# Kernel optimization log

Hardware: AMD Instinct MI355X
Metric: run time of the kernel (lower is better)

## Reference

```python
import jax, jax.numpy as jnp
import numpy as np
from jax.scipy.special import digamma

K = 3
N_CLASSES = 10
HIGH_CST = 1e7


def setup_inputs() -> dict:
    key = jax.random.key(0)
    k1, k2 = jax.random.split(key)
    X = jax.random.normal(k1, (8192, 128), dtype=jnp.float32)
    y = jax.random.randint(k2, (8192,), 0, N_CLASSES, dtype=jnp.int64)
    return {"X": X, "y": y}


def _pairwise_euclidean(X):
    sq = jnp.sum(X * X, axis=1)
    d2 = sq[:, None] - 2.0 * (X @ X.T) + sq[None, :]
    return jnp.sqrt(jnp.maximum(d2, 0.0))


def reference(X, y):
    N = X.shape[0]
    N_digamma = digamma(jnp.asarray(N, dtype=jnp.float32))

    # per-class counts N_x and weighted digamma average
    y32 = y.astype(jnp.int32)
    N_x = jnp.bincount(y32, length=N_CLASSES).astype(jnp.float32)
    avg_N_x = jnp.sum((N_x / N) * digamma(N_x))

    dists = _pairwise_euclidean(X)  # [N, N]

    # mask out different-class pairs with a huge constant
    same_class = y[:, None] == y[None, :]
    dists_same = jnp.where(same_class, dists, HIGH_CST)

    # k-th same-class neighbor distance (self included at distance 0 -> take k+1 smallest, last)
    neg_top, _ = jax.lax.top_k(-dists_same, K + 1)
    anchor_dists = -neg_top[:, -1]  # [N]

    # count all points (any class) within that radius, excluding self
    m_i = jnp.sum(dists <= anchor_dists[:, None], axis=1) - 1
    avg_m_i = jnp.mean(digamma(m_i.astype(jnp.float32)))

    k_digamma = digamma(jnp.asarray(K, dtype=jnp.float32))
    mi = N_digamma - avg_N_x + k_digamma - avg_m_i
    return jnp.maximum(mi / jnp.log(jnp.asarray(2.0, dtype=jnp.float32)), 0.0)
```

## Files before the change

kernel.cpp:

```cpp
#include <hip/hip_runtime.h>
#include <hip/hip_bf16.h>
#include <math.h>

#define NCLS 10
#define NTOT 8192
#define NS 64
#define NBLK2 544
#define NPMAX 9472
#define MAXSLOT 16
#define G1 2048

using short8 = __attribute__((ext_vector_type(8))) short;
using f32x4  = __attribute__((ext_vector_type(4))) float;

__device__ __forceinline__ float digammaf_dev(float x) {
    float r = 0.0f;
    while (x < 6.0f) { r -= 1.0f / x; x += 1.0f; }
    float inv = 1.0f / x;
    float inv2 = inv * inv;
    float s = logf(x) - 0.5f * inv
            - inv2 * (0.083333333333f - inv2 * (0.0083333333333f - inv2 * 0.0039682539683f));
    return r + s;
}

__device__ __forceinline__ void cmpswap(float& a, float& b) {
    float lo = fminf(a, b), hi = fmaxf(a, b);
    a = lo; b = hi;
}

__device__ __forceinline__ void ins7(float v, float& b0, float& b1, float& b2, float& b3) {
    float x0 = fminf(b0, v); float c0 = fmaxf(b0, v);
    float x1 = fminf(b1, c0); float c1 = fmaxf(b1, c0);
    float x2 = fminf(b2, c1); float c2 = fmaxf(b2, c1);
    float x3 = fminf(b3, c2);
    b0 = x0; b1 = x1; b2 = x2; b3 = x3;
}

__device__ __forceinline__ void bmerge(int mk, float& v0, float& v1, float& v2, float& v3) {
    float u0 = __shfl_xor(v0, mk), u1 = __shfl_xor(v1, mk);
    float u2 = __shfl_xor(v2, mk), u3 = __shfl_xor(v3, mk);
    float m0 = fminf(v0, u3), m1 = fminf(v1, u2);
    float m2 = fminf(v2, u1), m3 = fminf(v3, u0);
    cmpswap(m0, m2); cmpswap(m1, m3);
    cmpswap(m0, m1); cmpswap(m2, m3);
    v0 = m0; v1 = m1; v2 = m2; v3 = m3;
}

__device__ __forceinline__ void gload_lds16(const void* g, void* s) {
    __builtin_amdgcn_global_load_lds((const __attribute__((address_space(1))) void*)g,
                                     (__attribute__((address_space(3))) void*)s, 16, 0, 0);
}

__constant__ const int APn_[5] = {192, 0, 64, -1, -1};
__constant__ const int BPn_[5] = {64, 128, 192, 0, 64};

__global__ void prep_kernel(const float* __restrict__ X,
                            float* __restrict__ sq, unsigned short* __restrict__ XS) {
    int wave = threadIdx.x >> 6, lane = threadIdx.x & 63;
    int row = blockIdx.x * 4 + wave;
    float2 v = *(const float2*)(X + (size_t)row * 128 + lane * 2);
    __hip_bfloat16 h0 = __float2bfloat16(v.x);
    __hip_bfloat16 h1 = __float2bfloat16(v.y);
    float hf0 = __bfloat162float(h0), hf1 = __bfloat162float(h1);
    __hip_bfloat16 l0 = __float2bfloat16(v.x - hf0);
    __hip_bfloat16 l1 = __float2bfloat16(v.y - hf1);
    ushort2 hp, lp;
    hp.x = *(unsigned short*)&h0; hp.y = *(unsigned short*)&h1;
    lp.x = *(unsigned short*)&l0; lp.y = *(unsigned short*)&l1;
    *(ushort2*)(XS + (size_t)row * 256 + lane * 2) = hp;
    *(ushort2*)(XS + (size_t)row * 256 + 128 + lane * 2) = lp;
    float s = fmaf(v.x, v.x, v.y * v.y);
    #pragma unroll
    for (int off = 32; off > 0; off >>= 1) s += __shfl_down(s, off);
    if (lane == 0) sq[row] = s;
}

__global__ void count_kernel(const int* __restrict__ y, int* __restrict__ bcnt) {
    __shared__ int hist[NCLS];
    int t = threadIdx.x;
    if (t < NCLS) hist[t] = 0;
    __syncthreads();
    atomicAdd(&hist[y[blockIdx.x * 256 + t]], 1);
    __syncthreads();
    if (t < NCLS) bcnt[blockIdx.x * NCLS + t] = hist[t];
}

__global__ void plan_kernel(const int* __restrict__ bcnt, int* __restrict__ plan,
                            int* __restrict__ sOff, int* __restrict__ cls,
                            int* __restrict__ yP) {
    __shared__ int sT[NCLS], sBase[NCLS];
    const int c = threadIdx.x;
    for (int i = c; i < NPMAX; i += 256) yP[i] = -1;
    if (c < NCLS) {
        int run = 0;
        #pragma unroll 8
        for (int b = 0; b < 32; ++b) {
            sOff[b * NCLS + c] = run;
            run += bcnt[b * NCLS + c];
        }
        cls[c] = run;
        sT[c] = (run + 127) >> 7;
    }
    __syncthreads();
    if (c == 0) {
        int rowBase = 0, cum = 0;
        for (int q = 0; q < NCLS; ++q) {
            int T = sT[q];
            int nsl = (T > MAXSLOT) ? MAXSLOT : T;
            sBase[q] = rowBase;
            plan[q] = rowBase;
            plan[10 + q] = T;
            plan[20 + q] = nsl;
            plan[30 + q] = cum;
            rowBase += T << 7;
            cum += 2 * T * nsl;
        }
        plan[40] = cum;
    }
    __syncthreads();
    if (c < NCLS) {
        int rb = sBase[c];
        #pragma unroll 8
        for (int b = 0; b < 32; ++b) sOff[b * NCLS + c] += rb;
    }
}

__global__ void scatter_kernel(const int* __restrict__ y, const float* __restrict__ sq,
                               const unsigned short* __restrict__ XS,
                               const int* __restrict__ sOff,
                               unsigned short* __restrict__ XSP, float* __restrict__ sqP,
                               int* __restrict__ yP, int* __restrict__ idxP) {
    __shared__ int yloc[256];
    __shared__ int dstloc[256];
    const int b = blockIdx.x, t = threadIdx.x;
    const int gid = b * 256 + t;
    const int yv = y[gid];
    yloc[t] = yv;
    __syncthreads();
    int rank = 0;
    for (int k = 0; k < 256; ++k) rank += (k < t && yloc[k] == yv) ? 1 : 0;
    const int dst = sOff[b * NCLS + yv] + rank;
    dstloc[t] = dst;
    sqP[dst] = sq[gid];
    yP[dst] = yv;
    idxP[dst] = gid;
    __syncthreads();
    const int w = t >> 6, l = t & 63;
    for (int r = w; r < 256; r += 4) {
        int d = dstloc[r];
        *(ushort4*)(XSP + (size_t)d * 256 + l * 4) =
            *(const ushort4*)(XS + (size_t)(b * 256 + r) * 256 + l * 4);
    }
}

__global__ __launch_bounds__(256, 2)
void pass1_kernel(const unsigned short* __restrict__ XSP, const int* __restrict__ yP,
                  const float* __restrict__ sqP, const int* __restrict__ plan,
                  float* __restrict__ top4pP) {
    const int bid = blockIdx.x;
    if (bid >= plan[40]) return;
    __shared__ __align__(16) char smem[49152];

    const int t = threadIdx.x;
    const int w = t >> 6, l = t & 63;
    const int wr = w >> 1, wc = w & 1;
    const int lg = l >> 4, lo16 = l & 15;

    int cc = 0;
    #pragma unroll
    for (int q = 1; q < NCLS; ++q) if (bid >= plan[30 + q]) cc = q;
    const int rowBase = plan[cc], T = plan[10 + cc], nsl = plan[20 + cc];
    const int local = bid - plan[30 + cc];
    const int sIdx = local % nsl;
    const int itile2 = local / nsl;
    const int ibase = rowBase + (itile2 >> 1) * 128 + (itile2 & 1) * 64;

    float sqi[8]; int yi[8];
    #pragma unroll
    for (int mi = 0; mi < 2; ++mi)
        #pragma unroll
        for (int r = 0; r < 4; ++r) {
            int row = ibase + wr * 32 + mi * 16 + lg * 4 + r;
            sqi[mi * 4 + r] = sqP[row];
            yi[mi * 4 + r] = yP[row];
        }

    const int swz = (lo16 & 7) << 4;
    unsigned aoff[2], boff[2];
    #pragma unroll
    for (int kk = 0; kk < 2; ++kk) {
        const int cA = (kk * 64 + lg * 16) ^ swz;
        aoff[kk] = (unsigned)((wr * 32 + lo16) * 128 + cA);
        boff[kk] = (unsigned)(16384 + (wc * 64 + lo16) * 128 + cA);
    }
    const int scol = ((t & 7) ^ ((t >> 3) & 7)) << 3;
    const int srow = t >> 3;

    auto STAGE_A = [&](int panel, int par) {
        const unsigned short* g = XSP + (size_t)(ibase + srow) * 256 + panel + scol;
        char* d = smem + par * 8192 + t * 16;
        gload_lds16(g, d);
        gload_lds16(g + 32 * 256, d + 4096);
    };
    auto STAGE_B = [&](int jbase, int panel, int par) {
        const unsigned short* g = XSP + (size_t)(jbase + srow) * 256 + panel + scol;
        char* d = smem + 16384 + par * 16384 + t * 16;
        gload_lds16(g, d);
        gload_lds16(g + 32 * 256, d + 4096);
        gload_lds16(g + 64 * 256, d + 8192);
        gload_lds16(g + 96 * 256, d + 12288);
    };

    float tp0[8], tp1[8], tp2[8], tp3[8];
    #pragma unroll
    for (int c = 0; c < 8; ++c) {
        tp0[c] = 1e30f; tp1[c] = 1e30f; tp2[c] = 1e30f; tp3[c] = 1e30f;
    }

    STAGE_A(128, 0);
    STAGE_B(rowBase + sIdx * 128, 0, 0);
    __syncthreads();

    #pragma unroll 1
    for (int jt = sIdx; jt < T; jt += nsl) {
        const int jbase = rowBase + jt * 128;
        f32x4 accA[2][4], accB[2][4];
        f32x4 zz = {0.0f, 0.0f, 0.0f, 0.0f};
        #pragma unroll
        for (int mi = 0; mi < 2; ++mi)
            #pragma unroll
            for (int ni = 0; ni < 4; ++ni) { accA[mi][ni] = zz; accB[mi][ni] = zz; }

        #pragma unroll
        for (int s = 0; s < 6; ++s) {
            const int par = s & 1;
            if (s < 5) {
                if (APn_[s] >= 0) STAGE_A(APn_[s], (s + 1) & 1);
                STAGE_B(jbase, BPn_[s], (s + 1) & 1);
            } else if (jt + nsl < T) {
                STAGE_A(128, 0);
                STAGE_B(rowBase + (jt + nsl) * 128, 0, 0);
            }
            if (s == 4) {
                #pragma unroll
                for (int mi = 0; mi < 2; ++mi)
                    #pragma unroll
                    for (int ni = 0; ni < 4; ++ni) accB[mi][ni] = accB[mi][ni] + accA[mi][ni];
            }
            #pragma unroll
            for (int kk = 0; kk < 2; ++kk) {
                short8 aF[2], bF[4];
                #pragma unroll
                for (int mi = 0; mi < 2; ++mi)
                    aF[mi] = *(const short8*)(smem + par * 8192 + aoff[kk] + mi * 2048);
                #pragma unroll
                for (int ni = 0; ni < 4; ++ni)
                    bF[ni] = *(const short8*)(smem + boff[kk] + par * 16384 + ni * 2048);
                if (s < 2) {
                    #pragma unroll
                    for (int mi = 0; mi < 2; ++mi)
                        #pragma unroll
                        for (int ni = 0; ni < 4; ++ni)
                            accA[mi][ni] = __builtin_amdgcn_mfma_f32_16x16x32_bf16(
                                aF[mi], bF[ni], accA[mi][ni], 0, 0, 0);
                } else {
                    #pragma unroll
                    for (int mi = 0; mi < 2; ++mi)
                        #pragma unroll
                        for (int ni = 0; ni < 4; ++ni)
                            accB[mi][ni] = __builtin_amdgcn_mfma_f32_16x16x32_bf16(
                                aF[mi], bF[ni], accB[mi][ni], 0, 0, 0);
                }
            }
            __syncthreads();
        }

        float sqj[4]; int yj[4];
        #pragma unroll
        for (int ni = 0; ni < 4; ++ni) {
            int col = jbase + wc * 64 + ni * 16 + lo16;
            sqj[ni] = sqP[col];
            yj[ni] = yP[col];
        }
        #pragma unroll
        for (int mi = 0; mi < 2; ++mi)
            #pragma unroll
            for (int r = 0; r < 4; ++r) {
                const int idx = mi * 4 + r;
                #pragma unroll
                for (int ni = 0; ni < 4; ++ni) {
                    float d2 = fmaf(-2.0f, accB[mi][ni][r], sqi[idx] + sqj[ni]);
                    d2 = fmaxf(d2, 0.0f);
                    float v = (yi[idx] == yj[ni]) ? d2 : 1e30f;
                    ins7(v, tp0[idx], tp1[idx], tp2[idx], tp3[idx]);
                }
            }
    }

    float* scrR = (float*)smem;
    #pragma unroll
    for (int idx = 0; idx < 8; ++idx) {
        float v0 = tp0[idx], v1 = tp1[idx], v2 = tp2[idx], v3 = tp3[idx];
        bmerge(1, v0, v1, v2, v3); bmerge(2, v0, v1, v2, v3);
        bmerge(4, v0, v1, v2, v3); bmerge(8, v0, v1, v2, v3);
        if (lo16 == 0) {
            int rl = wr * 32 + (idx >> 2) * 16 + lg * 4 + (idx & 3);
            float4 st; st.x = v0; st.y = v1; st.z = v2; st.w = v3;
            *(float4*)(scrR + rl * 8 + wc * 4) = st;
        }
    }
    __syncthreads();
    if (t < 64) {
        float4 qa = *(float4*)(scrR + t * 8);
        float4 qb = *(float4*)(scrR + t * 8 + 4);
        float b0 = qa.x, b1 = qa.y, b2 = qa.z, b3 = qa.w;
        ins7(qb.x, b0, b1, b2, b3); ins7(qb.y, b0, b1, b2, b3);
        ins7(qb.z, b0, b1, b2, b3); ins7(qb.w, b0, b1, b2, b3);
        size_t base = ((size_t)(ibase + t) * MAXSLOT + sIdx) * 4;
        top4pP[base + 0] = b0; top4pP[base + 1] = b1;
        top4pP[base + 2] = b2; top4pP[base + 3] = b3;
    }
}

__global__ void anchorP_kernel(const float* __restrict__ top4pP, const int* __restrict__ yP,
                               const int* __restrict__ idxP, const int* __restrict__ plan,
                               float* __restrict__ anchor) {
    int r = blockIdx.x * 256 + threadIdx.x;
    int yv = yP[r];
    if (yv < 0) return;
    int nsl = plan[20 + yv];
    float b0 = 1e30f, b1 = 1e30f, b2 = 1e30f, b3 = 1e30f;
    const float4* q4 = (const float4*)(top4pP + (size_t)r * MAXSLOT * 4);
    for (int s = 0; s < nsl; ++s) {
        float4 q = q4[s];
        ins7(q.x, b0, b1, b2, b3); ins7(q.y, b0, b1, b2, b3);
        ins7(q.z, b0, b1, b2, b3); ins7(q.w, b0, b1, b2, b3);
    }
    anchor[idxP[r]] = b3;
}

__global__ __launch_bounds__(512, 4)
void pass2_kernel(const unsigned short* __restrict__ XS, const float* __restrict__ sq,
                  const float* __restrict__ anchor, int* __restrict__ cntp) {
    __shared__ __align__(16) char smem[65536];

    const int t = threadIdx.x;
    const int w = t >> 6, l = t & 63;
    const int wy = w >> 1, wx = w & 1;
    const int lg = l >> 4, lo16 = l & 15;

    const int bid = blockIdx.x;
    const int wg = (bid & 7) * (NBLK2 / 8) + (bid >> 3);
    int it = 0, rem = wg;
    while (rem >= 16 - (it >> 2)) { rem -= 16 - (it >> 2); ++it; }
    const int sIdx = (it >> 2) + rem;
    const int ibase = it * 128;
    const int jt_lo = (4 * sIdx < it) ? it : 4 * sIdx;
    const int jt_hi = 4 * sIdx + 3;

    float sqi[8], anc_i[8];
    #pragma unroll
    for (int mi = 0; mi < 2; ++mi)
        #pragma unroll
        for (int r = 0; r < 4; ++r) {
            int row = ibase + wy * 32 + mi * 16 + lg * 4 + r;
            sqi[mi * 4 + r] = sq[row];
            anc_i[mi * 4 + r] = anchor[row];
        }

    const int swz = (lo16 & 7) << 4;
    unsigned aoff[2], boff[2];
    #pragma unroll
    for (int kk = 0; kk < 2; ++kk) {
        const int cA = (kk * 64 + lg * 16) ^ swz;
        aoff[kk] = (unsigned)((wy * 32 + lo16) * 128 + cA);
        boff[kk] = (unsigned)(32768 + (wx * 64 + lo16) * 128 + cA);
    }
    const int scol = ((t & 7) ^ ((t >> 3) & 7)) << 3;
    const int srow = t >> 3;

    auto STAGE_A = [&](int panel, int par) {
        const unsigned short* g = XS + (size_t)(ibase + srow) * 256 + panel + scol;
        char* d = smem + par * 16384 + t * 16;
        gload_lds16(g, d);
        gload_lds16(g + 64 * 256, d + 8192);
    };
    auto STAGE_B = [&](int jbase, int panel, int par) {
        const unsigned short* g = XS + (size_t)(jbase + srow) * 256 + panel + scol;
        char* d = smem + 32768 + par * 16384 + t * 16;
        gload_lds16(g, d);
        gload_lds16(g + 64 * 256, d + 8192);
    };

    int rc[8];
    #pragma unroll
    for (int c = 0; c < 8; ++c) rc[c] = 0;

    STAGE_A(128, 0);
    STAGE_B(jt_lo * 128, 0, 0);
    __syncthreads();

    #pragma unroll 1
    for (int jt = jt_lo; jt <= jt_hi; ++jt) {
        const int jbase = jt * 128;
        const bool diag = (jt == it);
        f32x4 accA[2][4], accB[2][4];
        f32x4 zz = {0.0f, 0.0f, 0.0f, 0.0f};
        #pragma unroll
        for (int mi = 0; mi < 2; ++mi)
            #pragma unroll
            for (int ni = 0; ni < 4; ++ni) { accA[mi][ni] = zz; accB[mi][ni] = zz; }

        #pragma unroll
        for (int s = 0; s < 6; ++s) {
            const int par = s & 1;
            if (s < 5) {
                if (APn_[s] >= 0) STAGE_A(APn_[s], (s + 1) & 1);
                STAGE_B(jbase, BPn_[s], (s + 1) & 1);
            } else if (jt < jt_hi) {
                STAGE_A(128, 0);
                STAGE_B(jbase + 128, 0, 0);
            }
            if (s == 4) {
                #pragma unroll
                for (int mi = 0; mi < 2; ++mi)
                    #pragma unroll
                    for (int ni = 0; ni < 4; ++ni) accB[mi][ni] = accB[mi][ni] + accA[mi][ni];
            }
            #pragma unroll
            for (int kk = 0; kk < 2; ++kk) {
                short8 aF[2], bF[4];
                #pragma unroll
                for (int mi = 0; mi < 2; ++mi)
                    aF[mi] = *(const short8*)(smem + par * 16384 + aoff[kk] + mi * 2048);
                #pragma unroll
                for (int ni = 0; ni < 4; ++ni)
                    bF[ni] = *(const short8*)(smem + boff[kk] + par * 16384 + ni * 2048);
                if (s < 2) {
                    #pragma unroll
                    for (int mi = 0; mi < 2; ++mi)
                        #pragma unroll
                        for (int ni = 0; ni < 4; ++ni)
                            accA[mi][ni] = __builtin_amdgcn_mfma_f32_16x16x32_bf16(
                                aF[mi], bF[ni], accA[mi][ni], 0, 0, 0);
                } else {
                    #pragma unroll
                    for (int mi = 0; mi < 2; ++mi)
                        #pragma unroll
                        for (int ni = 0; ni < 4; ++ni)
                            accB[mi][ni] = __builtin_amdgcn_mfma_f32_16x16x32_bf16(
                                aF[mi], bF[ni], accB[mi][ni], 0, 0, 0);
                }
            }
            __syncthreads();
        }

        float sqj[4], anc_j[4];
        #pragma unroll
        for (int ni = 0; ni < 4; ++ni) {
            int col = jbase + wx * 64 + ni * 16 + lo16;
            sqj[ni] = sq[col];
            anc_j[ni] = anchor[col];
        }
        int colc[4] = {0, 0, 0, 0};
        #pragma unroll
        for (int mi = 0; mi < 2; ++mi)
            #pragma unroll
            for (int r = 0; r < 4; ++r) {
                const int idx = mi * 4 + r;
                #pragma unroll
                for (int ni = 0; ni < 4; ++ni) {
                    float d2 = fmaf(-2.0f, accB[mi][ni][r], sqi[idx] + sqj[ni]);
                    d2 = fmaxf(d2, 0.0f);
                    rc[idx] += (d2 <= anc_i[idx]) ? 1 : 0;
                    colc[ni] += (d2 <= anc_j[ni]) ? 1 : 0;
                }
            }
        if (!diag) {
            int* scrI = (int*)(smem + 49152);
            #pragma unroll
            for (int ni = 0; ni < 4; ++ni) {
                int c = colc[ni];
                c += __shfl_xor(c, 16); c += __shfl_xor(c, 32);
                if (lg == 0) scrI[(wx * 64 + ni * 16 + lo16) * 4 + wy] = c;
            }
            __syncthreads();
            if (t < 128)
                cntp[(size_t)(jbase + t) * NS + it] =
                    scrI[t * 4] + scrI[t * 4 + 1] + scrI[t * 4 + 2] + scrI[t * 4 + 3];
            __syncthreads();
        }
    }

    int* scr = (int*)smem;
    #pragma unroll
    for (int idx = 0; idx < 8; ++idx) {
        int c = rc[idx];
        c += __shfl_xor(c, 1); c += __shfl_xor(c, 2);
        c += __shfl_xor(c, 4); c += __shfl_xor(c, 8);
        if (lo16 == 0)
            scr[(wy * 32 + (idx >> 2) * 16 + lg * 4 + (idx & 3)) * 2 + wx] = c;
    }
    __syncthreads();
    const int slot_row = it + (sIdx - (it >> 2));
    if (t < 128) cntp[(size_t)(ibase + t) * NS + slot_row] = scr[t * 2] + scr[t * 2 + 1];
}

__global__ void reduce_kernel(const int* __restrict__ cntp, float* __restrict__ partials) {
    __shared__ float red[256];
    int t = threadIdx.x;
    int row = blockIdx.x * 256 + t;
    const int p = row >> 7;
    const int nvalid = p + 16 - (p >> 2);
    int s = 0;
    for (int c = 0; c < nvalid; ++c) s += cntp[(size_t)row * NS + c];
    red[t] = digammaf_dev((float)(s - 1));
    __syncthreads();
    for (int h = 128; h > 0; h >>= 1) {
        if (t < h) red[t] += red[t + h];
        __syncthreads();
    }
    if (t == 0) partials[blockIdx.x] = red[0];
}

__global__ void finalize_kernel(const float* __restrict__ partials, const int* __restrict__ cls,
                                float* __restrict__ out) {
    if (threadIdx.x == 0) {
        float acc = 0.0f;
        for (int c = 0; c < NTOT / 256; ++c) acc += partials[c];
        float Nf = (float)NTOT;
        float avg_m = acc / Nf;
        float avgNx = 0.0f;
        for (int c = 0; c < NCLS; ++c) {
            float nx = (float)cls[c];
            if (nx > 0.0f) avgNx += (nx / Nf) * digammaf_dev(nx);
        }
        float mi = digammaf_dev(Nf) - avgNx + digammaf_dev(3.0f) - avg_m;
        out[0] = fmaxf(mi / logf(2.0f), 0.0f);
    }
}

extern "C" void kernel_launch(void* const* d_in, const int* in_sizes, int n_in,
                              void* d_out, int out_size, void* d_ws, size_t ws_size,
                              hipStream_t stream) {
    const float* X = (const float*)d_in[0];
    const int* y = (const int*)d_in[1];
    float* out = (float*)d_out;

    float* sq       = (float*)d_ws;
    float* anchors  = sq + NTOT;
    float* partials = anchors + NTOT;
    int*   cls      = (int*)(partials + 32);
    int*   bcnt     = cls + 16;
    int*   sOff     = bcnt + 320;
    int*   plan     = sOff + 320;
    int*   yP       = plan + 48;
    int*   idxP     = yP + NPMAX;
    float* sqP      = (float*)(idxP + NPMAX);
    unsigned short* XS  = (unsigned short*)(sqP + NPMAX);
    unsigned short* XSP = XS + (size_t)NTOT * 256;
    float* top4pP   = (float*)(XSP + (size_t)NPMAX * 256);
    int*   cntp     = (int*)(top4pP + (size_t)NPMAX * MAXSLOT * 4);

    prep_kernel<<<NTOT / 4, 256, 0, stream>>>(X, sq, XS);
    count_kernel<<<NTOT / 256, 256, 0, stream>>>(y, bcnt);
    plan_kernel<<<1, 256, 0, stream>>>(bcnt, plan, sOff, cls, yP);
    scatter_kernel<<<NTOT / 256, 256, 0, stream>>>(y, sq, XS, sOff, XSP, sqP, yP, idxP);
    pass1_kernel<<<G1, 256, 0, stream>>>(XSP, yP, sqP, plan, top4pP);
    anchorP_kernel<<<NPMAX / 256, 256, 0, stream>>>(top4pP, yP, idxP, plan, anchors);
    pass2_kernel<<<NBLK2, 512, 0, stream>>>(XS, sq, anchors, cntp);
    reduce_kernel<<<NTOT / 256, 256, 0, stream>>>(cntp, partials);
    finalize_kernel<<<1, 64, 0, stream>>>(partials, cls, out);
}
```

Measured before the change: 149.1 us.

## Use 4-wave 256-thread blocks with 64x64 per-wave tiles in pass2

Restructures the pass2 distance-count GEMM from 8 waves of 32x64 tiles to 4 waves, each computing a 64x64 tile. This doubles MFMA work per fragment load and halves LDS fragment reads per output. It also changes the block-to-tile mapping order (column strip s then row tile). Staging is reorganised so each wave loads 32 rows with four 16-byte copies. The cost is higher register pressure from 16 accumulators times two sets, and fewer waves to hide latency.

```diff
diff --git a/kernel.cpp b/kernel.cpp
--- a/kernel.cpp
+++ b/kernel.cpp
@@ -339,31 +339,31 @@
     anchor[idxP[r]] = b3;
 }
 
-__global__ __launch_bounds__(512, 4)
+__global__ __launch_bounds__(256, 2)
 void pass2_kernel(const unsigned short* __restrict__ XS, const float* __restrict__ sq,
                   const float* __restrict__ anchor, int* __restrict__ cntp) {
     __shared__ __align__(16) char smem[65536];
 
     const int t = threadIdx.x;
     const int w = t >> 6, l = t & 63;
-    const int wy = w >> 1, wx = w & 1;
+    const int wr = w >> 1, wc = w & 1;
     const int lg = l >> 4, lo16 = l & 15;
 
     const int bid = blockIdx.x;
     const int wg = (bid & 7) * (NBLK2 / 8) + (bid >> 3);
-    int it = 0, rem = wg;
-    while (rem >= 16 - (it >> 2)) { rem -= 16 - (it >> 2); ++it; }
-    const int sIdx = (it >> 2) + rem;
+    int s = 0, rem = wg;
+    while (rem >= 4 * s + 4) { rem -= 4 * s + 4; ++s; }
+    const int it = rem;
     const int ibase = it * 128;
-    const int jt_lo = (4 * sIdx < it) ? it : 4 * sIdx;
-    const int jt_hi = 4 * sIdx + 3;
-
-    float sqi[8], anc_i[8];
-    #pragma unroll
-    for (int mi = 0; mi < 2; ++mi)
+    const int jt_lo = (it > 4 * s) ? it : 4 * s;
+    const int jt_hi = 4 * s + 3;
+
+    float sqi[16], anc_i[16];
+    #pragma unroll
+    for (int mi = 0; mi < 4; ++mi)
         #pragma unroll
         for (int r = 0; r < 4; ++r) {
-            int row = ibase + wy * 32 + mi * 16 + lg * 4 + r;
+            int row = ibase + wr * 64 + mi * 16 + lg * 4 + r;
             sqi[mi * 4 + r] = sq[row];
             anc_i[mi * 4 + r] = anchor[row];
         }
@@ -373,28 +373,31 @@
     #pragma unroll
     for (int kk = 0; kk < 2; ++kk) {
         const int cA = (kk * 64 + lg * 16) ^ swz;
-        aoff[kk] = (unsigned)((wy * 32 + lo16) * 128 + cA);
-        boff[kk] = (unsigned)(32768 + (wx * 64 + lo16) * 128 + cA);
-    }
-    const int scol = ((t & 7) ^ ((t >> 3) & 7)) << 3;
-    const int srow = t >> 3;
+        aoff[kk] = (unsigned)((wr * 64 + lo16) * 128 + cA);
+        boff[kk] = (unsigned)(32768 + (wc * 64 + lo16) * 128 + cA);
+    }
+    const int srow = w * 32 + (l >> 3);
+    const int scol = ((l & 7) ^ (l >> 3)) << 3;
+    const unsigned short* gsrc = XS + (size_t)srow * 256 + scol;
 
     auto STAGE_A = [&](int panel, int par) {
-        const unsigned short* g = XS + (size_t)(ibase + srow) * 256 + panel + scol;
-        char* d = smem + par * 16384 + t * 16;
-        gload_lds16(g, d);
-        gload_lds16(g + 64 * 256, d + 8192);
+        const unsigned short* gA = gsrc + (size_t)ibase * 256 + panel;
+        char* Ab = smem + par * 16384 + w * 4096;
+        #pragma unroll
+        for (int q = 0; q < 4; ++q)
+            gload_lds16(gA + (size_t)q * 8 * 256, Ab + q * 1024);
     };
     auto STAGE_B = [&](int jbase, int panel, int par) {
-        const unsigned short* g = XS + (size_t)(jbase + srow) * 256 + panel + scol;
-        char* d = smem + 32768 + par * 16384 + t * 16;
-        gload_lds16(g, d);
-        gload_lds16(g + 64 * 256, d + 8192);
+        const unsigned short* gB = gsrc + (size_t)jbase * 256 + panel;
+        char* Bb = smem + 32768 + par * 16384 + w * 4096;
+        #pragma unroll
+        for (int q = 0; q < 4; ++q)
+            gload_lds16(gB + (size_t)q * 8 * 256, Bb + q * 1024);
     };
 
-    int rc[8];
-    #pragma unroll
-    for (int c = 0; c < 8; ++c) rc[c] = 0;
+    int rc[16];
+    #pragma unroll
+    for (int c = 0; c < 16; ++c) rc[c] = 0;
 
     STAGE_A(128, 0);
     STAGE_B(jt_lo * 128, 0, 0);
@@ -404,48 +407,48 @@
     for (int jt = jt_lo; jt <= jt_hi; ++jt) {
         const int jbase = jt * 128;
         const bool diag = (jt == it);
-        f32x4 accA[2][4], accB[2][4];
+        f32x4 accA[4][4], accB[4][4];
         f32x4 zz = {0.0f, 0.0f, 0.0f, 0.0f};
         #pragma unroll
-        for (int mi = 0; mi < 2; ++mi)
+        for (int mi = 0; mi < 4; ++mi)
             #pragma unroll
             for (int ni = 0; ni < 4; ++ni) { accA[mi][ni] = zz; accB[mi][ni] = zz; }
 
         #pragma unroll
-        for (int s = 0; s < 6; ++s) {
-            const int par = s & 1;
-            if (s < 5) {
-                if (APn_[s] >= 0) STAGE_A(APn_[s], (s + 1) & 1);
-                STAGE_B(jbase, BPn_[s], (s + 1) & 1);
+        for (int st = 0; st < 6; ++st) {
+            const int par = st & 1;
+            if (st < 5) {
+                if (APn_[st] >= 0) STAGE_A(APn_[st], (st + 1) & 1);
+                STAGE_B(jbase, BPn_[st], (st + 1) & 1);
             } else if (jt < jt_hi) {
                 STAGE_A(128, 0);
                 STAGE_B(jbase + 128, 0, 0);
             }
-            if (s == 4) {
-                #pragma unroll
-                for (int mi = 0; mi < 2; ++mi)
+            if (st == 4) {
+                #pragma unroll
+                for (int mi = 0; mi < 4; ++mi)
                     #pragma unroll
                     for (int ni = 0; ni < 4; ++ni) accB[mi][ni] = accB[mi][ni] + accA[mi][ni];
             }
             #pragma unroll
             for (int kk = 0; kk < 2; ++kk) {
-                short8 aF[2], bF[4];
-                #pragma unroll
-                for (int mi = 0; mi < 2; ++mi)
+                short8 aF[4], bF[4];
+                #pragma unroll
+                for (int mi = 0; mi < 4; ++mi)
                     aF[mi] = *(const short8*)(smem + par * 16384 + aoff[kk] + mi * 2048);
                 #pragma unroll
                 for (int ni = 0; ni < 4; ++ni)
                     bF[ni] = *(const short8*)(smem + boff[kk] + par * 16384 + ni * 2048);
-                if (s < 2) {
+                if (st < 2) {
                     #pragma unroll
-                    for (int mi = 0; mi < 2; ++mi)
+                    for (int mi = 0; mi < 4; ++mi)
                         #pragma unroll
                         for (int ni = 0; ni < 4; ++ni)
                             accA[mi][ni] = __builtin_amdgcn_mfma_f32_16x16x32_bf16(
                                 aF[mi], bF[ni], accA[mi][ni], 0, 0, 0);
                 } else {
                     #pragma unroll
-                    for (int mi = 0; mi < 2; ++mi)
+                    for (int mi = 0; mi < 4; ++mi)
                         #pragma unroll
                         for (int ni = 0; ni < 4; ++ni)
                             accB[mi][ni] = __builtin_amdgcn_mfma_f32_16x16x32_bf16(
@@ -458,13 +461,13 @@
         float sqj[4], anc_j[4];
         #pragma unroll
         for (int ni = 0; ni < 4; ++ni) {
-            int col = jbase + wx * 64 + ni * 16 + lo16;
+            int col = jbase + wc * 64 + ni * 16 + lo16;
             sqj[ni] = sq[col];
             anc_j[ni] = anchor[col];
         }
         int colc[4] = {0, 0, 0, 0};
         #pragma unroll
-        for (int mi = 0; mi < 2; ++mi)
+        for (int mi = 0; mi < 4; ++mi)
             #pragma unroll
             for (int r = 0; r < 4; ++r) {
                 const int idx = mi * 4 + r;
@@ -482,27 +485,26 @@
             for (int ni = 0; ni < 4; ++ni) {
                 int c = colc[ni];
                 c += __shfl_xor(c, 16); c += __shfl_xor(c, 32);
-                if (lg == 0) scrI[(wx * 64 + ni * 16 + lo16) * 4 + wy] = c;
+                if (lg == 0) scrI[(wc * 64 + ni * 16 + lo16) * 2 + wr] = c;
             }
             __syncthreads();
             if (t < 128)
-                cntp[(size_t)(jbase + t) * NS + it] =
-                    scrI[t * 4] + scrI[t * 4 + 1] + scrI[t * 4 + 2] + scrI[t * 4 + 3];
+                cntp[(size_t)(jbase + t) * NS + it] = scrI[t * 2] + scrI[t * 2 + 1];
             __syncthreads();
         }
     }
 
     int* scr = (int*)smem;
     #pragma unroll
-    for (int idx = 0; idx < 8; ++idx) {
+    for (int idx = 0; idx < 16; ++idx) {
         int c = rc[idx];
         c += __shfl_xor(c, 1); c += __shfl_xor(c, 2);
         c += __shfl_xor(c, 4); c += __shfl_xor(c, 8);
         if (lo16 == 0)
-            scr[(wy * 32 + (idx >> 2) * 16 + lg * 4 + (idx & 3)) * 2 + wx] = c;
-    }
-    __syncthreads();
-    const int slot_row = it + (sIdx - (it >> 2));
+            scr[(wr * 64 + (idx >> 2) * 16 + lg * 4 + (idx & 3)) * 2 + wc] = c;
+    }
+    __syncthreads();
+    const int slot_row = it + (s - (it >> 2));
     if (t < 128) cntp[(size_t)(ibase + t) * NS + slot_row] = scr[t * 2] + scr[t * 2 + 1];
 }
 
@@ -568,7 +570,7 @@
     scatter_kernel<<<NTOT / 256, 256, 0, stream>>>(y, sq, XS, sOff, XSP, sqP, yP, idxP);
     pass1_kernel<<<G1, 256, 0, stream>>>(XSP, yP, sqP, plan, top4pP);
     anchorP_kernel<<<NPMAX / 256, 256, 0, stream>>>(top4pP, yP, idxP, plan, anchors);
-    pass2_kernel<<<NBLK2, 512, 0, stream>>>(XS, sq, anchors, cntp);
+    pass2_kernel<<<NBLK2, 256, 0, stream>>>(XS, sq, anchors, cntp);
     reduce_kernel<<<NTOT / 256, 256, 0, stream>>>(cntp, partials);
     finalize_kernel<<<1, 64, 0, stream>>>(partials, cls, out);
 }
```

New measurement: 153.3 us. +2.8%, slower.
